# Kernel optimization log

Hardware: AMD Instinct MI355X
Metric: run time of the kernel (lower is better)

Reference implementation:

```python
import jax, jax.numpy as jnp
import numpy as np
from jax import lax

THETA = 0.7
DN = ('NCHW', 'OIHW', 'NCHW')


def setup_inputs() -> dict:
    key = jax.random.key(0)
    k1, k2 = jax.random.split(key)
    x = jax.random.normal(k1, (16, 64, 128, 128), dtype=jnp.float32)
    W = jax.random.normal(k2, (64, 64, 3, 3), dtype=jnp.float32) * 0.05
    return {"x": x, "W": W}


def _shift_sum(x):
    # Sum of the center view plus the 8 shifted views of the reflection-padded
    # input (the original code's lt/mt/rt/lm/center/mr/ld/md/rd slices cover
    # exactly the full 3x3 neighborhood of the padded tensor).
    B, C, H, W_ = x.shape
    xp = jnp.pad(x, ((0, 0), (0, 0), (1, 1), (1, 1)), mode='reflect')
    s = jnp.zeros_like(x)
    for dy in range(3):
        for dx in range(3):
            s = s + xp[:, :, dy:dy + H, dx:dx + W_]
    return s


def reference(x, W):
    # Conv is linear and bias=False, so sum_i conv(shift_i(x)) == conv(sum_i shift_i(x)).
    s = _shift_sum(x)  # [B,C,H,W]
    out_normal = lax.conv_general_dilated(s, W, (1, 1), [(1, 1), (1, 1)], dimension_numbers=DN)
    kernel_diff = W.sum(axis=(2, 3))[:, :, None, None]  # [C_out,C_in,1,1]
    out_diff = lax.conv_general_dilated(s, kernel_diff, (1, 1), [(0, 0), (0, 0)], dimension_numbers=DN)
    return out_normal - THETA * out_diff
```

## Files before the change

### kernel.cpp

```cpp
#include <hip/hip_runtime.h>
#include <stdint.h>


#define THETA 0.7f

typedef __attribute__((ext_vector_type(8))) short bf16x8;
typedef __attribute__((ext_vector_type(16))) float f32x16;

__device__ inline unsigned short f2bf(float f) {
    unsigned u = __float_as_uint(f);
    u = (u + 0x7FFFu + ((u >> 16) & 1u)) >> 16;
    return (unsigned short)u;
}
__device__ inline unsigned cvt_pk_bf16(float lo, float hi) {
    unsigned r;
    asm volatile("v_cvt_pk_bf16_f32 %0, %1, %2" : "=v"(r) : "v"(lo), "v"(hi));
    return r;
}

__global__ void weff_kernel(const float* __restrict__ W, unsigned short* __restrict__ Wt2) {
    int t = blockIdx.x * blockDim.x + threadIdx.x;
    if (t >= 512) return;
    int o = t >> 3;
    int ch8 = t & 7;
    int c0 = ch8 * 8;
    int ic = ch8 >> 1;
    int mf = o >> 5;
    int lane = (o & 31) | ((ch8 & 1) << 5);

    float v[8][9];
    float tsum[8];
#pragma unroll
    for (int j = 0; j < 8; j++) {
        const float* w = W + ((size_t)o * 64 + c0 + j) * 9;
        float sum = 0.f;
#pragma unroll
        for (int k = 0; k < 9; k++) { v[j][k] = w[k]; sum += v[j][k]; }
        tsum[j] = sum;
    }
#pragma unroll
    for (int tap = 0; tap < 9; tap++) {
        unsigned short* dst = Wt2 + (((size_t)(tap * 4 + ic) * 2 + mf) * 64 + lane) * 8;
#pragma unroll
        for (int j = 0; j < 8; j++) {
            float val = v[j][tap] - ((tap == 4) ? THETA * tsum[j] : 0.f);
            dst[j] = f2bf(val);
        }
    }
}

__global__ __launch_bounds__(512, 4) void fused_kernel(const float* __restrict__ x,
                                                       const unsigned short* __restrict__ Wt2,
                                                       float* __restrict__ out) {
    __shared__ __align__(16) unsigned short sS[4 * 132 * 64];

    int bid0 = blockIdx.x;
    int bid = (bid0 & 7) * 128 + (bid0 >> 3);
    int b = bid >> 6;
    int h0 = (bid & 63) * 2;
    int tid = threadIdx.x;
    int lane = tid & 63;
    int wv = tid >> 6;
    int n32 = lane & 31;
    int q2 = lane >> 5;
    int ohalf = wv >> 2;
    int orow = (wv >> 1) & 1;
    int whalf = wv & 1;

    int4 z = make_int4(0, 0, 0, 0);
    if (tid < 64) {
        int rr = tid >> 4;
        int sl = ((tid >> 3) & 1) ? 129 : 0;
        int g = tid & 7;
        *(int4*)((char*)sS + ((size_t)(rr * 132 + sl) * 8 + g) * 16) = z;
    }
    if (h0 == 0)
        for (int i = tid; i < 1056; i += 512) *(int4*)((char*)sS + (size_t)i * 16) = z;
    if (h0 == 126)
        for (int i = tid; i < 1056; i += 512) *(int4*)((char*)sS + (size_t)(3168 + i) * 16) = z;

    {
        int w4 = tid & 31;
        int cg = tid >> 5;
        int c0 = cg * 4;
        int u8 = cg >> 1;
        int hh = (cg & 1) * 4;
        const float* xp = x + ((size_t)(b * 64 + c0)) * 16384 + w4 * 4;

        int hgf = (h0 == 0) ? 0 : h0 - 1;
        int hm = (hgf == 0) ? 1 : hgf - 1;
        float4 A[4], Bv[4], C[4];
#pragma unroll
        for (int cc = 0; cc < 4; cc++) {
            A[cc]  = *(const float4*)(xp + (size_t)cc * 16384 + (size_t)hm * 128);
            Bv[cc] = *(const float4*)(xp + (size_t)cc * 16384 + (size_t)hgf * 128);
            C[cc]  = *(const float4*)(xp + (size_t)cc * 16384 + (size_t)(hgf + 1) * 128);
        }

#pragma unroll
        for (int rr = 0; rr < 4; rr++) {
            int hg = h0 - 1 + rr;
            if (hg < 0 || hg > 127) continue;

            float4 Cn[4];
            if (rr < 3) {
                int hn = hg + 2;
                if (hn > 127) hn = 126;
#pragma unroll
                for (int cc = 0; cc < 4; cc++)
                    Cn[cc] = *(const float4*)(xp + (size_t)cc * 16384 + (size_t)hn * 128);
            }

            float rf[4][4];
#pragma unroll
            for (int cc = 0; cc < 4; cc++) {
                float4 vs;
                vs.x = A[cc].x + Bv[cc].x + C[cc].x;
                vs.y = A[cc].y + Bv[cc].y + C[cc].y;
                vs.z = A[cc].z + Bv[cc].z + C[cc].z;
                vs.w = A[cc].w + Bv[cc].w + C[cc].w;
                float L = __shfl_up(vs.w, 1, 32);
                float R = __shfl_down(vs.x, 1, 32);
                rf[cc][0] = (w4 == 0) ? vs.x + 2.f * vs.y : L + vs.x + vs.y;
                rf[cc][1] = vs.x + vs.y + vs.z;
                rf[cc][2] = vs.y + vs.z + vs.w;
                rf[cc][3] = (w4 == 31) ? 2.f * vs.z + vs.w : vs.z + vs.w + R;
            }
#pragma unroll
            for (int k = 0; k < 4; k++) {
                int slot = w4 * 4 + k + 1;
                uint2 o2 = make_uint2(cvt_pk_bf16(rf[0][k], rf[1][k]),
                                      cvt_pk_bf16(rf[2][k], rf[3][k]));
                int p = u8 ^ (slot & 7) ^ ((slot >> 2) & 7);
                *(uint2*)(sS + (size_t)(rr * 132 + slot) * 64 + (p << 3) + hh) = o2;
            }
            if (rr < 3) {
#pragma unroll
                for (int cc = 0; cc < 4; cc++) { A[cc] = Bv[cc]; Bv[cc] = C[cc]; C[cc] = Cn[cc]; }
            }
        }
    }
    __syncthreads();

    int p0[3][4];
#pragma unroll
    for (int kx = 0; kx < 3; kx++)
#pragma unroll
        for (int ic = 0; ic < 4; ic++) {
            int slot = n32 + kx + whalf * 64;
            int g = (ic * 2 + q2) ^ (slot & 7) ^ ((slot >> 2) & 7);
            p0[kx][ic] = slot * 64 + g * 8;
        }

    f32x16 acc[2];
#pragma unroll
    for (int nf = 0; nf < 2; nf++)
#pragma unroll
        for (int r = 0; r < 16; r++) acc[nf][r] = 0.f;

    bf16x8 Af[4], An[4], B0[4], B0n[4], B1[4];
#pragma unroll
    for (int ic = 0; ic < 4; ic++) {
        Af[ic] = *(const bf16x8*)(Wt2 + (((size_t)(0 * 4 + ic) * 2 + ohalf) * 64 + lane) * 8);
        B0[ic] = *(const bf16x8*)(sS + (size_t)(orow + 0) * 8448 + p0[0][ic]);
    }

#pragma unroll
    for (int tap = 0; tap < 9; tap++) {
        int ky = tap / 3, kx = tap % 3;
        const unsigned short* brow = sS + (size_t)(orow + ky) * 8448;
#pragma unroll
        for (int ic = 0; ic < 4; ic++)
            B1[ic] = *(const bf16x8*)(brow + p0[kx][ic] + 2048);
        if (tap < 8) {
            int kyn = (tap + 1) / 3, kxn = (tap + 1) % 3;
            const unsigned short* brn = sS + (size_t)(orow + kyn) * 8448;
#pragma unroll
            for (int ic = 0; ic < 4; ic++) {
                B0n[ic] = *(const bf16x8*)(brn + p0[kxn][ic]);
                An[ic] = *(const bf16x8*)(Wt2 + (((size_t)((tap + 1) * 4 + ic) * 2 + ohalf) * 64 + lane) * 8);
            }
        }
#pragma unroll
        for (int ic = 0; ic < 4; ic++)
            acc[0] = __builtin_amdgcn_mfma_f32_32x32x16_bf16(Af[ic], B0[ic], acc[0], 0, 0, 0);
#pragma unroll
        for (int ic = 0; ic < 4; ic++)
            acc[1] = __builtin_amdgcn_mfma_f32_32x32x16_bf16(Af[ic], B1[ic], acc[1], 0, 0, 0);
        if (tap < 8) {
#pragma unroll
            for (int k = 0; k < 4; k++) { Af[k] = An[k]; B0[k] = B0n[k]; }
        }
    }

    float* ob = out + ((size_t)b * 64) * 16384 + (size_t)(h0 + orow) * 128 + whalf * 64;
#pragma unroll
    for (int nf = 0; nf < 2; nf++)
#pragma unroll
        for (int r = 0; r < 16; r++) {
            int o = ohalf * 32 + (r & 3) + 8 * (r >> 2) + 4 * q2;
            ob[(size_t)o * 16384 + nf * 32 + n32] = acc[nf][r];
        }
}

extern "C" void kernel_launch(void* const* d_in, const int* in_sizes, int n_in,
                              void* d_out, int out_size, void* d_ws, size_t ws_size,
                              hipStream_t stream) {
    const float* x = (const float*)d_in[0];
    const float* W = (const float*)d_in[1];
    float* outp = (float*)d_out;

    unsigned short* Wt2 = (unsigned short*)d_ws;

    weff_kernel<<<2, 256, 0, stream>>>(W, Wt2);
    fused_kernel<<<1024, 512, 0, stream>>>(x, Wt2, outp);
}
```

Measured before the change: 136.4 us.

## Process two row strips per block and prefetch second strip's rows during first conv

Each block now handles four output rows as two sequential strips of two rows, halving the grid. The global loads for the second strip's first three input rows are issued before the first strip's MFMA convolution, so their latency can overlap with compute. The change also amortizes per-block setup across two strips. In exchange it adds extra barriers, keeps more registers live during the first conv, and halves the number of blocks available to fill the GPU.

```diff
diff --git a/kernel.cpp b/kernel.cpp
--- a/kernel.cpp
+++ b/kernel.cpp
@@ -49,15 +49,120 @@
     }
 }
 
+__device__ __forceinline__ void stage_rows(unsigned short* __restrict__ sS,
+                                           const float* __restrict__ xp,
+                                           int h0, int w4, int u8, int hh,
+                                           float4 A[4], float4 Bv[4], float4 C[4]) {
+#pragma unroll
+    for (int rr = 0; rr < 4; rr++) {
+        int hg = h0 - 1 + rr;
+        if (hg < 0 || hg > 127) continue;
+
+        float4 Cn[4];
+        if (rr < 3) {
+            int hn = hg + 2;
+            if (hn > 127) hn = 126;
+#pragma unroll
+            for (int cc = 0; cc < 4; cc++)
+                Cn[cc] = *(const float4*)(xp + (size_t)cc * 16384 + (size_t)hn * 128);
+        }
+
+        float rf[4][4];
+#pragma unroll
+        for (int cc = 0; cc < 4; cc++) {
+            float4 vs;
+            vs.x = A[cc].x + Bv[cc].x + C[cc].x;
+            vs.y = A[cc].y + Bv[cc].y + C[cc].y;
+            vs.z = A[cc].z + Bv[cc].z + C[cc].z;
+            vs.w = A[cc].w + Bv[cc].w + C[cc].w;
+            float L = __shfl_up(vs.w, 1, 32);
+            float R = __shfl_down(vs.x, 1, 32);
+            rf[cc][0] = (w4 == 0) ? vs.x + 2.f * vs.y : L + vs.x + vs.y;
+            rf[cc][1] = vs.x + vs.y + vs.z;
+            rf[cc][2] = vs.y + vs.z + vs.w;
+            rf[cc][3] = (w4 == 31) ? 2.f * vs.z + vs.w : vs.z + vs.w + R;
+        }
+#pragma unroll
+        for (int k = 0; k < 4; k++) {
+            int slot = w4 * 4 + k + 1;
+            uint2 o2 = make_uint2(cvt_pk_bf16(rf[0][k], rf[1][k]),
+                                  cvt_pk_bf16(rf[2][k], rf[3][k]));
+            int p = u8 ^ (slot & 7) ^ ((slot >> 2) & 7);
+            *(uint2*)(sS + (size_t)(rr * 132 + slot) * 64 + (p << 3) + hh) = o2;
+        }
+        if (rr < 3) {
+#pragma unroll
+            for (int cc = 0; cc < 4; cc++) { A[cc] = Bv[cc]; Bv[cc] = C[cc]; C[cc] = Cn[cc]; }
+        }
+    }
+}
+
+__device__ __forceinline__ void conv_strip(const unsigned short* __restrict__ sS,
+                                           const unsigned short* __restrict__ Wt2,
+                                           float* __restrict__ out,
+                                           int b, int h0, int lane, int orow,
+                                           int ohalf, int whalf, int n32, int q2,
+                                           const int (*p0)[4]) {
+    f32x16 acc[2];
+#pragma unroll
+    for (int nf = 0; nf < 2; nf++)
+#pragma unroll
+        for (int r = 0; r < 16; r++) acc[nf][r] = 0.f;
+
+    bf16x8 Af[4], An[4], B0[4], B0n[4], B1[4];
+#pragma unroll
+    for (int ic = 0; ic < 4; ic++) {
+        Af[ic] = *(const bf16x8*)(Wt2 + (((size_t)(0 * 4 + ic) * 2 + ohalf) * 64 + lane) * 8);
+        B0[ic] = *(const bf16x8*)(sS + (size_t)(orow + 0) * 8448 + p0[0][ic]);
+    }
+
+#pragma unroll
+    for (int tap = 0; tap < 9; tap++) {
+        int ky = tap / 3, kx = tap % 3;
+        const unsigned short* brow = sS + (size_t)(orow + ky) * 8448;
+#pragma unroll
+        for (int ic = 0; ic < 4; ic++)
+            B1[ic] = *(const bf16x8*)(brow + p0[kx][ic] + 2048);
+        if (tap < 8) {
+            int kyn = (tap + 1) / 3, kxn = (tap + 1) % 3;
+            const unsigned short* brn = sS + (size_t)(orow + kyn) * 8448;
+#pragma unroll
+            for (int ic = 0; ic < 4; ic++) {
+                B0n[ic] = *(const bf16x8*)(brn + p0[kxn][ic]);
+                An[ic] = *(const bf16x8*)(Wt2 + (((size_t)((tap + 1) * 4 + ic) * 2 + ohalf) * 64 + lane) * 8);
+            }
+        }
+#pragma unroll
+        for (int ic = 0; ic < 4; ic++)
+            acc[0] = __builtin_amdgcn_mfma_f32_32x32x16_bf16(Af[ic], B0[ic], acc[0], 0, 0, 0);
+#pragma unroll
+        for (int ic = 0; ic < 4; ic++)
+            acc[1] = __builtin_amdgcn_mfma_f32_32x32x16_bf16(Af[ic], B1[ic], acc[1], 0, 0, 0);
+        if (tap < 8) {
+#pragma unroll
+            for (int k = 0; k < 4; k++) { Af[k] = An[k]; B0[k] = B0n[k]; }
+        }
+    }
+
+    float* ob = out + ((size_t)b * 64) * 16384 + (size_t)(h0 + orow) * 128 + whalf * 64;
+#pragma unroll
+    for (int nf = 0; nf < 2; nf++)
+#pragma unroll
+        for (int r = 0; r < 16; r++) {
+            int o = ohalf * 32 + (r & 3) + 8 * (r >> 2) + 4 * q2;
+            ob[(size_t)o * 16384 + nf * 32 + n32] = acc[nf][r];
+        }
+}
+
 __global__ __launch_bounds__(512, 4) void fused_kernel(const float* __restrict__ x,
                                                        const unsigned short* __restrict__ Wt2,
                                                        float* __restrict__ out) {
     __shared__ __align__(16) unsigned short sS[4 * 132 * 64];
 
     int bid0 = blockIdx.x;
-    int bid = (bid0 & 7) * 128 + (bid0 >> 3);
-    int b = bid >> 6;
-    int h0 = (bid & 63) * 2;
+    int bid = (bid0 & 7) * 64 + (bid0 >> 3);
+    int b = bid >> 5;
+    int base = (bid & 31) * 4;
     int tid = threadIdx.x;
     int lane = tid & 63;
     int wv = tid >> 6;
@@ -67,6 +172,12 @@
     int orow = (wv >> 1) & 1;
     int whalf = wv & 1;
 
+    int w4 = tid & 31;
+    int cg = tid >> 5;
+    int u8 = cg >> 1;
+    int hh = (cg & 1) * 4;
+    const float* xp = x + ((size_t)(b * 64 + cg * 4)) * 16384 + w4 * 4;
+
     int4 z = make_int4(0, 0, 0, 0);
     if (tid < 64) {
         int rr = tid >> 4;
@@ -74,19 +185,11 @@
         int g = tid & 7;
         *(int4*)((char*)sS + ((size_t)(rr * 132 + sl) * 8 + g) * 16) = z;
     }
+
+    int h0 = base;
     if (h0 == 0)
         for (int i = tid; i < 1056; i += 512) *(int4*)((char*)sS + (size_t)i * 16) = z;
-    if (h0 == 126)
-        for (int i = tid; i < 1056; i += 512) *(int4*)((char*)sS + (size_t)(3168 + i) * 16) = z;
-
     {
-        int w4 = tid & 31;
-        int cg = tid >> 5;
-        int c0 = cg * 4;
-        int u8 = cg >> 1;
-        int hh = (cg & 1) * 4;
-        const float* xp = x + ((size_t)(b * 64 + c0)) * 16384 + w4 * 4;
-
         int hgf = (h0 == 0) ? 0 : h0 - 1;
         int hm = (hgf == 0) ? 1 : hgf - 1;
         float4 A[4], Bv[4], C[4];
@@ -96,51 +199,19 @@
             Bv[cc] = *(const float4*)(xp + (size_t)cc * 16384 + (size_t)hgf * 128);
             C[cc]  = *(const float4*)(xp + (size_t)cc * 16384 + (size_t)(hgf + 1) * 128);
         }
-
-#pragma unroll
-        for (int rr = 0; rr < 4; rr++) {
-            int hg = h0 - 1 + rr;
-            if (hg < 0 || hg > 127) continue;
-
-            float4 Cn[4];
-            if (rr < 3) {
-                int hn = hg + 2;
-                if (hn > 127) hn = 126;
-#pragma unroll
-                for (int cc = 0; cc < 4; cc++)
-                    Cn[cc] = *(const float4*)(xp + (size_t)cc * 16384 + (size_t)hn * 128);
-            }
-
-            float rf[4][4];
-#pragma unroll
-            for (int cc = 0; cc < 4; cc++) {
-                float4 vs;
-                vs.x = A[cc].x + Bv[cc].x + C[cc].x;
-                vs.y = A[cc].y + Bv[cc].y + C[cc].y;
-                vs.z = A[cc].z + Bv[cc].z + C[cc].z;
-                vs.w = A[cc].w + Bv[cc].w + C[cc].w;
-                float L = __shfl_up(vs.w, 1, 32);
-                float R = __shfl_down(vs.x, 1, 32);
-                rf[cc][0] = (w4 == 0) ? vs.x + 2.f * vs.y : L + vs.x + vs.y;
-                rf[cc][1] = vs.x + vs.y + vs.z;
-                rf[cc][2] = vs.y + vs.z + vs.w;
-                rf[cc][3] = (w4 == 31) ? 2.f * vs.z + vs.w : vs.z + vs.w + R;
-            }
-#pragma unroll
-            for (int k = 0; k < 4; k++) {
-                int slot = w4 * 4 + k + 1;
-                uint2 o2 = make_uint2(cvt_pk_bf16(rf[0][k], rf[1][k]),
-                                      cvt_pk_bf16(rf[2][k], rf[3][k]));
-                int p = u8 ^ (slot & 7) ^ ((slot >> 2) & 7);
-                *(uint2*)(sS + (size_t)(rr * 132 + slot) * 64 + (p << 3) + hh) = o2;
-            }
-            if (rr < 3) {
-#pragma unroll
-                for (int cc = 0; cc < 4; cc++) { A[cc] = Bv[cc]; Bv[cc] = C[cc]; C[cc] = Cn[cc]; }
-            }
-        }
+        stage_rows(sS, xp, h0, w4, u8, hh, A, Bv, C);
     }
     __syncthreads();
+
+    int h0b = base + 2;
+    float4 PA[4], PB[4], PC[4];
+#pragma unroll
+    for (int cc = 0; cc < 4; cc++) {
+        PA[cc] = *(const float4*)(xp + (size_t)cc * 16384 + (size_t)(h0b - 2) * 128);
+        PB[cc] = *(const float4*)(xp + (size_t)cc * 16384 + (size_t)(h0b - 1) * 128);
+        PC[cc] = *(const float4*)(xp + (size_t)cc * 16384 + (size_t)h0b * 128);
+    }
+    __builtin_amdgcn_sched_barrier(0);
 
     int p0[3][4];
 #pragma unroll
@@ -152,55 +223,15 @@
             p0[kx][ic] = slot * 64 + g * 8;
         }
 
-    f32x16 acc[2];
-#pragma unroll
-    for (int nf = 0; nf < 2; nf++)
-#pragma unroll
-        for (int r = 0; r < 16; r++) acc[nf][r] = 0.f;
-
-    bf16x8 Af[4], An[4], B0[4], B0n[4], B1[4];
-#pragma unroll
-    for (int ic = 0; ic < 4; ic++) {
-        Af[ic] = *(const bf16x8*)(Wt2 + (((size_t)(0 * 4 + ic) * 2 + ohalf) * 64 + lane) * 8);
-        B0[ic] = *(const bf16x8*)(sS + (size_t)(orow + 0) * 8448 + p0[0][ic]);
-    }
-
-#pragma unroll
-    for (int tap = 0; tap < 9; tap++) {
-        int ky = tap / 3, kx = tap % 3;
-        const unsigned short* brow = sS + (size_t)(orow + ky) * 8448;
-#pragma unroll
-        for (int ic = 0; ic < 4; ic++)
-            B1[ic] = *(const bf16x8*)(brow + p0[kx][ic] + 2048);
-        if (tap < 8) {
-            int kyn = (tap + 1) / 3, kxn = (tap + 1) % 3;
-            const unsigned short* brn = sS + (size_t)(orow + kyn) * 8448;
-#pragma unroll
-            for (int ic = 0; ic < 4; ic++) {
-                B0n[ic] = *(const bf16x8*)(brn + p0[kxn][ic]);
-                An[ic] = *(const bf16x8*)(Wt2 + (((size_t)((tap + 1) * 4 + ic) * 2 + ohalf) * 64 + lane) * 8);
-            }
-        }
-#pragma unroll
-        for (int ic = 0; ic < 4; ic++)
-            acc[0] = __builtin_amdgcn_mfma_f32_32x32x16_bf16(Af[ic], B0[ic], acc[0], 0, 0, 0);
-#pragma unroll
-        for (int ic = 0; ic < 4; ic++)
-            acc[1] = __builtin_amdgcn_mfma_f32_32x32x16_bf16(Af[ic], B1[ic], acc[1], 0, 0, 0);
-        if (tap < 8) {
-#pragma unroll
-            for (int k = 0; k < 4; k++) { Af[k] = An[k]; B0[k] = B0n[k]; }
-        }
-    }
-
-    float* ob = out + ((size_t)b * 64) * 16384 + (size_t)(h0 + orow) * 128 + whalf * 64;
-#pragma unroll
-    for (int nf = 0; nf < 2; nf++)
-#pragma unroll
-        for (int r = 0; r < 16; r++) {
-            int o = ohalf * 32 + (r & 3) + 8 * (r >> 2) + 4 * q2;
-            ob[(size_t)o * 16384 + nf * 32 + n32] = acc[nf][r];
-        }
+    conv_strip(sS, Wt2, out, b, h0, lane, orow, ohalf, whalf, n32, q2, p0);
+    __syncthreads();
+
+    if (h0b == 126)
+        for (int i = tid; i < 1056; i += 512) *(int4*)((char*)sS + (size_t)(3168 + i) * 16) = z;
+    stage_rows(sS, xp, h0b, w4, u8, hh, PA, PB, PC);
+    __syncthreads();
+
+    conv_strip(sS, Wt2, out, b, h0b, lane, orow, ohalf, whalf, n32, q2, p0);
 }
 
 extern "C" void kernel_launch(void* const* d_in, const int* in_sizes, int n_in,
@@ -213,5 +244,5 @@
     unsigned short* Wt2 = (unsigned short*)d_ws;
 
     weff_kernel<<<2, 256, 0, stream>>>(W, Wt2);
-    fused_kernel<<<1024, 512, 0, stream>>>(x, Wt2, outp);
-}
+    fused_kernel<<<512, 512, 0, stream>>>(x, Wt2, outp);
+}
```

Measured after the change: 186.1 us. 36.4% more time.
